# Kernel optimization log

Measured on AMD Instinct MI355X. Metric: run time of the kernel, lower is better.

Reference implementation:

```python
import jax, jax.numpy as jnp
import numpy as np


def setup_inputs() -> dict:
    key = jax.random.key(0)
    ks = jax.random.split(key, 8)
    B, N, D = 8, 2048, 128
    s = 1.0 / float(np.sqrt(D))
    node = jax.random.normal(ks[0], (B, N, D), dtype=jnp.float32)
    node_mask = jax.random.randint(ks[1], (B, N), 0, 2, dtype=jnp.int32)
    punctuation_graph = jax.random.randint(ks[2], (B, N, N), 0, 2, dtype=jnp.int32)
    w_nw = jax.random.uniform(ks[3], (1, D), jnp.float32, -s, s)
    b_nw = jax.random.uniform(ks[4], (1,), jnp.float32, -s, s)
    w_self = jax.random.uniform(ks[5], (D, D), jnp.float32, -s, s)
    b_self = jax.random.uniform(ks[6], (D,), jnp.float32, -s, s)
    w_punct = jax.random.uniform(ks[7], (D, D), jnp.float32, -s, s)
    return {"node": node, "node_mask": node_mask, "punctuation_graph": punctuation_graph,
            "w_nw": w_nw, "b_nw": b_nw, "w_self": w_self, "b_self": b_self,
            "w_punct": w_punct, "iteration_steps": 2}


def reference(node, node_mask, punctuation_graph, w_nw, b_nw, w_self, b_self, w_punct, iteration_steps):
    B, N, D = node.shape
    # dd_graph = mask outer product with zeroed diagonal; graph = dd_graph * punctuation_graph
    eye = jnp.eye(N, dtype=punctuation_graph.dtype)
    dd = node_mask[:, None, :] * node_mask[:, :, None] * (1 - eye)[None, :, :]  # [B,N,N]
    graph = dd * punctuation_graph  # [B,N,N] int, binary
    nbr_num = graph.sum(-1)  # [B,N]
    # replace_masked_values(nbr_num, nbr_num>=1, 1): nodes with no neighbors get denom 1
    nbr_f = jnp.where(nbr_num >= 1, nbr_num.astype(node.dtype), jnp.asarray(1.0, node.dtype))
    gmask = graph > 0
    weights = []
    x = node
    for _ in range(iteration_steps):  # small fixed step count
        dw = jax.nn.sigmoid(jnp.einsum('bnd,od->bno', x, w_nw) + b_nw)[..., 0]  # [B,N]
        weights.append(dw)
        self_info = jnp.einsum('bnd,ed->bne', x, w_self) + b_self  # [B,N,D]
        info_p = jnp.einsum('bnd,ed->bne', x, w_punct)  # [B,N,D]
        # node_weight[b,i,j] = dw[b,j] where graph[b,i,j] else 0
        nw = jnp.where(gmask, dw[:, None, :], jnp.asarray(0.0, x.dtype))  # [B,N,N]
        agg = jnp.einsum('bnm,bmd->bnd', nw, info_p) / nbr_f[..., None]
        x = jax.nn.relu(self_info + agg)
    all_weight = jnp.stack(weights, axis=1)  # [B, steps, N]
    return x, all_weight
```

## Files before the change

### kernel.cpp

```cpp
#include <hip/hip_runtime.h>
#include <hip/hip_bf16.h>

#define BB 8
#define NN 2048
#define DD 128

typedef __attribute__((ext_vector_type(8))) __bf16 bf16x8;
typedef __attribute__((ext_vector_type(4))) float f32x4;
typedef __attribute__((ext_vector_type(4))) int   i32x4;

static __device__ __forceinline__ unsigned short f2bf(float f) {
    union { float f; unsigned u; } v; v.f = f;
    unsigned r = (v.u + 0x7FFFu + ((v.u >> 16) & 1u)) >> 16;
    return (unsigned short)r;
}
static __device__ __forceinline__ float bf2f(unsigned short b) {
    union { unsigned u; float f; } v; v.u = ((unsigned)b) << 16;
    return v.f;
}

__global__ __launch_bounds__(256) void kernP(
    const int* __restrict__ punct, const int* __restrict__ mask,
    unsigned* __restrict__ pk, float* __restrict__ scale_g, float* __restrict__ pdm_g)
{
    const int t = threadIdx.x;
    const int wave = t >> 6, lane = t & 63;
    const int row_g = blockIdx.x * 4 + wave;
    const int b = row_g >> 11;
    const int i = row_g & (NN - 1);

    const int* prow = punct + (size_t)row_g * NN;
    const int* mrow = mask + (size_t)b * NN;

    unsigned pk0 = 0, pk1 = 0;
    int acc = 0;
    #pragma unroll 4
    for (int w = 0; w < 32; ++w) {
        const int col = w * 64 + lane;
        const int p = prow[col];
        const int m = mrow[col];
        const int pred = (p & m) & 1;
        unsigned long long bal = __ballot(pred);
        if (lane == w) { pk0 = (unsigned)bal; pk1 = (unsigned)(bal >> 32); }
        acc += pred + ((col == i ? pred : 0) << 16);
    }
    #pragma unroll
    for (int o = 32; o > 0; o >>= 1) acc += __shfl_xor(acc, o, 64);

    if (lane < 32) {
        uint2 w2; w2.x = pk0; w2.y = pk1;
        *(uint2*)(pk + (size_t)row_g * 64 + 2 * lane) = w2;
    }

    if (lane == 0) {
        const int nall = acc & 0xFFFF;
        const int pdm  = acc >> 16;
        const int mi   = mrow[i];
        const int nbr  = nall - pdm;
        scale_g[row_g] = mi ? 1.f / (float)(nbr < 1 ? 1 : nbr) : 0.f;
        pdm_g[row_g]   = (float)pdm;
    }
}

__global__ __launch_bounds__(256) void kernB(
    const float* __restrict__ x,
    const float* __restrict__ w_nw,  const float* __restrict__ b_nw,
    const float* __restrict__ w_self,const float* __restrict__ b_self,
    const float* __restrict__ w_punct,
    float* __restrict__ si_out,
    unsigned short* __restrict__ yne_out,
    unsigned short* __restrict__ yT_out,
    float* __restrict__ aw_out)
{
    __shared__ unsigned short xt[64*32];
    __shared__ unsigned short wst[128*32];
    __shared__ unsigned short wpt[128*32];
    __shared__ float wnw_l[DD];
    __shared__ float red[256];
    __shared__ float dw_l[64];
    __shared__ unsigned short ytl[128*72];

    const int t  = threadIdx.x;
    const int n0 = blockIdx.x * 64;
    const int b  = n0 >> 11;
    const int nb = n0 & (NN - 1);

    if (t < DD) wnw_l[t] = w_nw[t];
    __syncthreads();

    const int wave = t >> 6, lane = t & 63;
    const int wm = wave >> 1, wn = wave & 1;
    const int quad = lane >> 4, l16 = lane & 15;

    const int n_loc = t >> 2, dq = t & 3;
    const int we = t >> 1,   wh = t & 1;

    f32x4 accs[2][4] = {}; f32x4 accp[2][4] = {};
    float dwpart = 0.f;

    #pragma unroll
    for (int kk = 0; kk < 4; ++kk) {
        const int k0 = kk * 32;
        {
            const float* xs = x + (size_t)(n0 + n_loc) * DD + k0 + dq * 8;
            f32x4 a = *(const f32x4*)xs;
            f32x4 c = *(const f32x4*)(xs + 4);
            const float* wv = &wnw_l[k0 + dq * 8];
            dwpart += a.x*wv[0] + a.y*wv[1] + a.z*wv[2] + a.w*wv[3]
                    + c.x*wv[4] + c.y*wv[5] + c.z*wv[6] + c.w*wv[7];
            unsigned q0 = f2bf(a.x) | ((unsigned)f2bf(a.y) << 16);
            unsigned q1 = f2bf(a.z) | ((unsigned)f2bf(a.w) << 16);
            unsigned q2 = f2bf(c.x) | ((unsigned)f2bf(c.y) << 16);
            unsigned q3 = f2bf(c.z) | ((unsigned)f2bf(c.w) << 16);
            i32x4 pw = {(int)q0,(int)q1,(int)q2,(int)q3};
            *(i32x4*)&xt[n_loc*32 + dq*8] = pw;
        }
        {
            const float* s1 = w_self  + (size_t)we * DD + k0 + wh*16;
            const float* s2 = w_punct + (size_t)we * DD + k0 + wh*16;
            f32x4 a0 = *(const f32x4*)s1;      f32x4 a1 = *(const f32x4*)(s1+4);
            f32x4 a2 = *(const f32x4*)(s1+8);  f32x4 a3 = *(const f32x4*)(s1+12);
            unsigned q0 = f2bf(a0.x) | ((unsigned)f2bf(a0.y)<<16);
            unsigned q1 = f2bf(a0.z) | ((unsigned)f2bf(a0.w)<<16);
            unsigned q2 = f2bf(a1.x) | ((unsigned)f2bf(a1.y)<<16);
            unsigned q3 = f2bf(a1.z) | ((unsigned)f2bf(a1.w)<<16);
            unsigned q4 = f2bf(a2.x) | ((unsigned)f2bf(a2.y)<<16);
            unsigned q5 = f2bf(a2.z) | ((unsigned)f2bf(a2.w)<<16);
            unsigned q6 = f2bf(a3.x) | ((unsigned)f2bf(a3.y)<<16);
            unsigned q7 = f2bf(a3.z) | ((unsigned)f2bf(a3.w)<<16);
            i32x4 pw0 = {(int)q0,(int)q1,(int)q2,(int)q3};
            i32x4 pw1 = {(int)q4,(int)q5,(int)q6,(int)q7};
            *(i32x4*)&wst[we*32 + wh*16]     = pw0;
            *(i32x4*)&wst[we*32 + wh*16 + 8] = pw1;
            f32x4 c0 = *(const f32x4*)s2;      f32x4 c1 = *(const f32x4*)(s2+4);
            f32x4 c2 = *(const f32x4*)(s2+8);  f32x4 c3 = *(const f32x4*)(s2+12);
            unsigned r0 = f2bf(c0.x) | ((unsigned)f2bf(c0.y)<<16);
            unsigned r1 = f2bf(c0.z) | ((unsigned)f2bf(c0.w)<<16);
            unsigned r2 = f2bf(c1.x) | ((unsigned)f2bf(c1.y)<<16);
            unsigned r3 = f2bf(c1.z) | ((unsigned)f2bf(c1.w)<<16);
            unsigned r4 = f2bf(c2.x) | ((unsigned)f2bf(c2.y)<<16);
            unsigned r5 = f2bf(c2.z) | ((unsigned)f2bf(c2.w)<<16);
            unsigned r6 = f2bf(c3.x) | ((unsigned)f2bf(c3.y)<<16);
            unsigned r7 = f2bf(c3.z) | ((unsigned)f2bf(c3.w)<<16);
            i32x4 pv0 = {(int)r0,(int)r1,(int)r2,(int)r3};
            i32x4 pv1 = {(int)r4,(int)r5,(int)r6,(int)r7};
            *(i32x4*)&wpt[we*32 + wh*16]     = pv0;
            *(i32x4*)&wpt[we*32 + wh*16 + 8] = pv1;
        }
        __syncthreads();
        bf16x8 af[2], bs[4], bp[4];
        #pragma unroll
        for (int mt = 0; mt < 2; ++mt)
            af[mt] = *(const bf16x8*)&xt[(wm*32 + mt*16 + l16)*32 + quad*8];
        #pragma unroll
        for (int nt = 0; nt < 4; ++nt) {
            const int er = wn*64 + nt*16 + l16;
            bs[nt] = *(const bf16x8*)&wst[er*32 + quad*8];
            bp[nt] = *(const bf16x8*)&wpt[er*32 + quad*8];
        }
        #pragma unroll
        for (int mt = 0; mt < 2; ++mt)
            #pragma unroll
            for (int nt = 0; nt < 4; ++nt) {
                accs[mt][nt] = __builtin_amdgcn_mfma_f32_16x16x32_bf16(af[mt], bs[nt], accs[mt][nt], 0, 0, 0);
                accp[mt][nt] = __builtin_amdgcn_mfma_f32_16x16x32_bf16(af[mt], bp[nt], accp[mt][nt], 0, 0, 0);
            }
        __syncthreads();
    }

    red[t] = dwpart;
    __syncthreads();
    if (t < 64) {
        float s = red[4*t] + red[4*t+1] + red[4*t+2] + red[4*t+3] + b_nw[0];
        float dv = 1.f / (1.f + __expf(-s));
        dw_l[t] = dv;
        aw_out[(size_t)b * 2 * NN + nb + t] = dv;
    }
    __syncthreads();

    #pragma unroll
    for (int mt = 0; mt < 2; ++mt) {
        #pragma unroll
        for (int nt = 0; nt < 4; ++nt) {
            const int e = wn*64 + nt*16 + l16;
            const float bsv = b_self[e];
            #pragma unroll
            for (int r = 0; r < 4; ++r) {
                const int nl = wm*32 + mt*16 + quad*4 + r;
                const size_t idx = (size_t)(n0 + nl) * DD + e;
                si_out[idx] = accs[mt][nt][r] + bsv;
                const float yv = dw_l[nl] * accp[mt][nt][r];
                const unsigned short ub = f2bf(yv);
                yne_out[idx] = ub;
                ytl[e*72 + nl] = ub;
            }
        }
    }
    __syncthreads();
    {
        const int e = t >> 1, half = t & 1;
        const i32x4* src = (const i32x4*)&ytl[e*72 + half*32];
        i32x4 v0 = src[0], v1 = src[1], v2 = src[2], v3 = src[3];
        i32x4* dst = (i32x4*)(yT_out + (size_t)(b*DD + e) * NN + nb + half*32);
        dst[0] = v0; dst[1] = v1; dst[2] = v2; dst[3] = v3;
    }
}

__global__ __launch_bounds__(256) void kernC(
    const unsigned* __restrict__ pk,
    const float* __restrict__ scale_g, const float* __restrict__ pdm_g,
    const unsigned short* __restrict__ yT,
    const float* __restrict__ si,
    const unsigned short* __restrict__ yne,
    float* __restrict__ x_out)
{
    __shared__ unsigned pPk[64 * 68];
    __shared__ float scale_l[64];
    __shared__ float pdm_l[64];

    const int t  = threadIdx.x;
    const int b  = blockIdx.x >> 5;
    const int i0 = (blockIdx.x & 31) * 64;
    const size_t rg0 = (size_t)b * NN + i0;

    #pragma unroll
    for (int r = 0; r < 4; ++r) {
        const int u   = r * 256 + t;
        const int row = u >> 4;
        const int wq  = (u & 15) * 4;
        i32x4 v = *(const i32x4*)(pk + (rg0 + row) * 64 + wq);
        *(i32x4*)&pPk[row * 68 + wq] = v;
    }
    if (t < 64) {
        scale_l[t] = scale_g[rg0 + t];
        pdm_l[t]   = pdm_g[rg0 + t];
    }
    __syncthreads();

    const int wn = t >> 6, lane = t & 63;
    const int quad = lane >> 4, l16 = lane & 15;
    const unsigned short* yTb = yT + (size_t)b * DD * NN;

    f32x4 acc[4][2] = {};

    #pragma unroll 4
    for (int kk = 0; kk < 64; ++kk) {
        bf16x8 bfr[2];
        #pragma unroll
        for (int nt = 0; nt < 2; ++nt) {
            const int e = wn*32 + nt*16 + l16;
            bfr[nt] = *(const bf16x8*)(yTb + (size_t)e * NN + kk*32 + quad*8);
        }
        bf16x8 af[4];
        #pragma unroll
        for (int mt = 0; mt < 4; ++mt) {
            const unsigned w = pPk[(mt*16 + l16) * 68 + kk];
            const unsigned by = (w >> (quad * 8)) & 0xFFu;
            i32x4 ex;
            ex.x = ((by &   1u) ? 0x3F80 : 0) | ((by &   2u) ? 0x3F800000 : 0);
            ex.y = ((by &   4u) ? 0x3F80 : 0) | ((by &   8u) ? 0x3F800000 : 0);
            ex.z = ((by &  16u) ? 0x3F80 : 0) | ((by &  32u) ? 0x3F800000 : 0);
            ex.w = ((by &  64u) ? 0x3F80 : 0) | ((by & 128u) ? 0x3F800000 : 0);
            union { i32x4 i; bf16x8 h; } cv; cv.i = ex;
            af[mt] = cv.h;
        }
        #pragma unroll
        for (int mt = 0; mt < 4; ++mt)
            #pragma unroll
            for (int nt = 0; nt < 2; ++nt)
                acc[mt][nt] = __builtin_amdgcn_mfma_f32_16x16x32_bf16(af[mt], bfr[nt], acc[mt][nt], 0, 0, 0);
    }

    #pragma unroll
    for (int mt = 0; mt < 4; ++mt) {
        #pragma unroll
        for (int nt = 0; nt < 2; ++nt) {
            const int e = wn*32 + nt*16 + l16;
            #pragma unroll
            for (int r = 0; r < 4; ++r) {
                const int row = mt*16 + quad*4 + r;
                const size_t idx = (rg0 + row) * DD + e;
                const float yv = bf2f(yne[idx]);
                float v = si[idx] + scale_l[row] * (acc[mt][nt][r] - pdm_l[row] * yv);
                x_out[idx] = fmaxf(v, 0.f);
            }
        }
    }
}

extern "C" void kernel_launch(void* const* d_in, const int* in_sizes, int n_in,
                              void* d_out, int out_size, void* d_ws, size_t ws_size,
                              hipStream_t stream) {
    const float* node   = (const float*)d_in[0];
    const int*   mask   = (const int*)  d_in[1];
    const int*   punct  = (const int*)  d_in[2];
    const float* w_nw   = (const float*)d_in[3];
    const float* b_nw   = (const float*)d_in[4];
    const float* w_self = (const float*)d_in[5];
    const float* b_self = (const float*)d_in[6];
    const float* w_punct= (const float*)d_in[7];

    float* xout = (float*)d_out;
    float* aw   = xout + (size_t)BB * NN * DD;

    char* w = (char*)d_ws;
    float*          si   = (float*)w;
    unsigned short* yne  = (unsigned short*)(w + (8u  << 20));
    unsigned short* yT   = (unsigned short*)(w + (12u << 20));
    unsigned*       pk   = (unsigned*)(w + (16u << 20));
    float*          scl  = (float*)(w + (20u << 20));
    float*          pdm  = (float*)(w + (20u << 20) + (64u << 10));

    dim3 blk(256);
    kernP<<<dim3(4096), blk, 0, stream>>>(punct, mask, pk, scl, pdm);
    kernB<<<dim3(256), blk, 0, stream>>>(node, w_nw, b_nw, w_self, b_self, w_punct,
                                         si, yne, yT, aw);
    kernC<<<dim3(256), blk, 0, stream>>>(pk, scl, pdm, yT, si, yne, xout);
    kernB<<<dim3(256), blk, 0, stream>>>(xout, w_nw, b_nw, w_self, b_self, w_punct,
                                         si, yne, yT, aw + NN);
    kernC<<<dim3(256), blk, 0, stream>>>(pk, scl, pdm, yT, si, yne, xout);
}
```

Before: 286.3 us.

## Reassociate aggregation to multiply graph by dw-scaled x before weight projection, fusing steps

Reorders the per-step math: the graph aggregation now runs on dw-scaled x instead of on x@W_punct, and the self and punct projections are fused into one K=256 GEMM over [x, aggregate] against a concatenated bf16 weight matrix. That matrix is converted once in an extra kernP block. Each step's output kernel also emits the next step's bf16 x, scaled x, transposed operand and dw, which removes the separate projection kernel for step two and the fp32 self_info round trip. The trade-off is extra bf16 rounding of the aggregate before the projection, one more sync-heavy epilogue per block, and a redundant dummy dw computation in the final step.

```diff
diff --git a/kernel.cpp b/kernel.cpp
--- a/kernel.cpp
+++ b/kernel.cpp
@@ -21,9 +21,20 @@
 
 __global__ __launch_bounds__(256) void kernP(
     const int* __restrict__ punct, const int* __restrict__ mask,
-    unsigned* __restrict__ pk, float* __restrict__ scale_g, float* __restrict__ pdm_g)
+    const float* __restrict__ w_self, const float* __restrict__ w_punct,
+    unsigned* __restrict__ pk, float* __restrict__ scale_g, float* __restrict__ pdm_g,
+    unsigned short* __restrict__ wc)
 {
     const int t = threadIdx.x;
+    if (blockIdx.x == 4096) {
+        for (int idx = t; idx < 128 * 256; idx += 256) {
+            const int e = idx >> 8, k = idx & 255;
+            const float v = (k < 128) ? w_self[e * 128 + k]
+                                      : w_punct[e * 128 + (k - 128)];
+            wc[idx] = f2bf(v);
+        }
+        return;
+    }
     const int wave = t >> 6, lane = t & 63;
     const int row_g = blockIdx.x * 4 + wave;
     const int b = row_g >> 11;
@@ -37,9 +48,7 @@
     #pragma unroll 4
     for (int w = 0; w < 32; ++w) {
         const int col = w * 64 + lane;
-        const int p = prow[col];
-        const int m = mrow[col];
-        const int pred = (p & m) & 1;
+        const int pred = (prow[col] & mrow[col]) & 1;
         unsigned long long bal = __ballot(pred);
         if (lane == w) { pk0 = (unsigned)bal; pk1 = (unsigned)(bal >> 32); }
         acc += pred + ((col == i ? pred : 0) << 16);
@@ -51,7 +60,6 @@
         uint2 w2; w2.x = pk0; w2.y = pk1;
         *(uint2*)(pk + (size_t)row_g * 64 + 2 * lane) = w2;
     }
-
     if (lane == 0) {
         const int nall = acc & 0xFFFF;
         const int pdm  = acc >> 16;
@@ -62,23 +70,17 @@
     }
 }
 
-__global__ __launch_bounds__(256) void kernB(
+__global__ __launch_bounds__(256) void kernD(
     const float* __restrict__ x,
-    const float* __restrict__ w_nw,  const float* __restrict__ b_nw,
-    const float* __restrict__ w_self,const float* __restrict__ b_self,
-    const float* __restrict__ w_punct,
-    float* __restrict__ si_out,
-    unsigned short* __restrict__ yne_out,
-    unsigned short* __restrict__ yT_out,
-    float* __restrict__ aw_out)
+    const float* __restrict__ w_nw, const float* __restrict__ b_nw,
+    float* __restrict__ aw_out,
+    unsigned short* __restrict__ xbf, unsigned short* __restrict__ xw,
+    unsigned short* __restrict__ xwT)
 {
-    __shared__ unsigned short xt[64*32];
-    __shared__ unsigned short wst[128*32];
-    __shared__ unsigned short wpt[128*32];
     __shared__ float wnw_l[DD];
     __shared__ float red[256];
     __shared__ float dw_l[64];
-    __shared__ unsigned short ytl[128*72];
+    __shared__ unsigned short xl[64 * 136];
 
     const int t  = threadIdx.x;
     const int n0 = blockIdx.x * 64;
@@ -88,87 +90,18 @@
     if (t < DD) wnw_l[t] = w_nw[t];
     __syncthreads();
 
-    const int wave = t >> 6, lane = t & 63;
-    const int wm = wave >> 1, wn = wave & 1;
-    const int quad = lane >> 4, l16 = lane & 15;
-
-    const int n_loc = t >> 2, dq = t & 3;
-    const int we = t >> 1,   wh = t & 1;
-
-    f32x4 accs[2][4] = {}; f32x4 accp[2][4] = {};
-    float dwpart = 0.f;
-
-    #pragma unroll
-    for (int kk = 0; kk < 4; ++kk) {
-        const int k0 = kk * 32;
-        {
-            const float* xs = x + (size_t)(n0 + n_loc) * DD + k0 + dq * 8;
-            f32x4 a = *(const f32x4*)xs;
-            f32x4 c = *(const f32x4*)(xs + 4);
-            const float* wv = &wnw_l[k0 + dq * 8];
-            dwpart += a.x*wv[0] + a.y*wv[1] + a.z*wv[2] + a.w*wv[3]
-                    + c.x*wv[4] + c.y*wv[5] + c.z*wv[6] + c.w*wv[7];
-            unsigned q0 = f2bf(a.x) | ((unsigned)f2bf(a.y) << 16);
-            unsigned q1 = f2bf(a.z) | ((unsigned)f2bf(a.w) << 16);
-            unsigned q2 = f2bf(c.x) | ((unsigned)f2bf(c.y) << 16);
-            unsigned q3 = f2bf(c.z) | ((unsigned)f2bf(c.w) << 16);
-            i32x4 pw = {(int)q0,(int)q1,(int)q2,(int)q3};
-            *(i32x4*)&xt[n_loc*32 + dq*8] = pw;
-        }
-        {
-            const float* s1 = w_self  + (size_t)we * DD + k0 + wh*16;
-            const float* s2 = w_punct + (size_t)we * DD + k0 + wh*16;
-            f32x4 a0 = *(const f32x4*)s1;      f32x4 a1 = *(const f32x4*)(s1+4);
-            f32x4 a2 = *(const f32x4*)(s1+8);  f32x4 a3 = *(const f32x4*)(s1+12);
-            unsigned q0 = f2bf(a0.x) | ((unsigned)f2bf(a0.y)<<16);
-            unsigned q1 = f2bf(a0.z) | ((unsigned)f2bf(a0.w)<<16);
-            unsigned q2 = f2bf(a1.x) | ((unsigned)f2bf(a1.y)<<16);
-            unsigned q3 = f2bf(a1.z) | ((unsigned)f2bf(a1.w)<<16);
-            unsigned q4 = f2bf(a2.x) | ((unsigned)f2bf(a2.y)<<16);
-            unsigned q5 = f2bf(a2.z) | ((unsigned)f2bf(a2.w)<<16);
-            unsigned q6 = f2bf(a3.x) | ((unsigned)f2bf(a3.y)<<16);
-            unsigned q7 = f2bf(a3.z) | ((unsigned)f2bf(a3.w)<<16);
-            i32x4 pw0 = {(int)q0,(int)q1,(int)q2,(int)q3};
-            i32x4 pw1 = {(int)q4,(int)q5,(int)q6,(int)q7};
-            *(i32x4*)&wst[we*32 + wh*16]     = pw0;
-            *(i32x4*)&wst[we*32 + wh*16 + 8] = pw1;
-            f32x4 c0 = *(const f32x4*)s2;      f32x4 c1 = *(const f32x4*)(s2+4);
-            f32x4 c2 = *(const f32x4*)(s2+8);  f32x4 c3 = *(const f32x4*)(s2+12);
-            unsigned r0 = f2bf(c0.x) | ((unsigned)f2bf(c0.y)<<16);
-            unsigned r1 = f2bf(c0.z) | ((unsigned)f2bf(c0.w)<<16);
-            unsigned r2 = f2bf(c1.x) | ((unsigned)f2bf(c1.y)<<16);
-            unsigned r3 = f2bf(c1.z) | ((unsigned)f2bf(c1.w)<<16);
-            unsigned r4 = f2bf(c2.x) | ((unsigned)f2bf(c2.y)<<16);
-            unsigned r5 = f2bf(c2.z) | ((unsigned)f2bf(c2.w)<<16);
-            unsigned r6 = f2bf(c3.x) | ((unsigned)f2bf(c3.y)<<16);
-            unsigned r7 = f2bf(c3.z) | ((unsigned)f2bf(c3.w)<<16);
-            i32x4 pv0 = {(int)r0,(int)r1,(int)r2,(int)r3};
-            i32x4 pv1 = {(int)r4,(int)r5,(int)r6,(int)r7};
-            *(i32x4*)&wpt[we*32 + wh*16]     = pv0;
-            *(i32x4*)&wpt[we*32 + wh*16 + 8] = pv1;
-        }
-        __syncthreads();
-        bf16x8 af[2], bs[4], bp[4];
-        #pragma unroll
-        for (int mt = 0; mt < 2; ++mt)
-            af[mt] = *(const bf16x8*)&xt[(wm*32 + mt*16 + l16)*32 + quad*8];
-        #pragma unroll
-        for (int nt = 0; nt < 4; ++nt) {
-            const int er = wn*64 + nt*16 + l16;
-            bs[nt] = *(const bf16x8*)&wst[er*32 + quad*8];
-            bp[nt] = *(const bf16x8*)&wpt[er*32 + quad*8];
-        }
-        #pragma unroll
-        for (int mt = 0; mt < 2; ++mt)
-            #pragma unroll
-            for (int nt = 0; nt < 4; ++nt) {
-                accs[mt][nt] = __builtin_amdgcn_mfma_f32_16x16x32_bf16(af[mt], bs[nt], accs[mt][nt], 0, 0, 0);
-                accp[mt][nt] = __builtin_amdgcn_mfma_f32_16x16x32_bf16(af[mt], bp[nt], accp[mt][nt], 0, 0, 0);
-            }
-        __syncthreads();
-    }
-
-    red[t] = dwpart;
+    const int row = t >> 2, q = t & 3;
+    const float* xs = x + (size_t)(n0 + row) * DD + q * 32;
+    float vals[32];
+    float dp = 0.f;
+    #pragma unroll
+    for (int j = 0; j < 8; ++j) {
+        f32x4 a = *(const f32x4*)(xs + j * 4);
+        vals[j*4+0] = a.x; vals[j*4+1] = a.y; vals[j*4+2] = a.z; vals[j*4+3] = a.w;
+        const float* wv = &wnw_l[q * 32 + j * 4];
+        dp += a.x*wv[0] + a.y*wv[1] + a.z*wv[2] + a.w*wv[3];
+    }
+    red[t] = dp;
     __syncthreads();
     if (t < 64) {
         float s = red[4*t] + red[4*t+1] + red[4*t+2] + red[4*t+3] + b_nw[0];
@@ -178,45 +111,66 @@
     }
     __syncthreads();
 
-    #pragma unroll
-    for (int mt = 0; mt < 2; ++mt) {
-        #pragma unroll
-        for (int nt = 0; nt < 4; ++nt) {
-            const int e = wn*64 + nt*16 + l16;
-            const float bsv = b_self[e];
-            #pragma unroll
-            for (int r = 0; r < 4; ++r) {
-                const int nl = wm*32 + mt*16 + quad*4 + r;
-                const size_t idx = (size_t)(n0 + nl) * DD + e;
-                si_out[idx] = accs[mt][nt][r] + bsv;
-                const float yv = dw_l[nl] * accp[mt][nt][r];
-                const unsigned short ub = f2bf(yv);
-                yne_out[idx] = ub;
-                ytl[e*72 + nl] = ub;
-            }
-        }
-    }
-    __syncthreads();
-    {
-        const int e = t >> 1, half = t & 1;
-        const i32x4* src = (const i32x4*)&ytl[e*72 + half*32];
-        i32x4 v0 = src[0], v1 = src[1], v2 = src[2], v3 = src[3];
-        i32x4* dst = (i32x4*)(yT_out + (size_t)(b*DD + e) * NN + nb + half*32);
-        dst[0] = v0; dst[1] = v1; dst[2] = v2; dst[3] = v3;
-    }
-}
-
-__global__ __launch_bounds__(256) void kernC(
+    unsigned pb[16];
+    #pragma unroll
+    for (int j = 0; j < 16; ++j)
+        pb[j] = f2bf(vals[2*j]) | ((unsigned)f2bf(vals[2*j+1]) << 16);
+    {
+        i32x4* dst = (i32x4*)(xbf + (size_t)(n0 + row) * DD + q * 32);
+        i32x4 v0 = {(int)pb[0],(int)pb[1],(int)pb[2],(int)pb[3]};
+        i32x4 v1 = {(int)pb[4],(int)pb[5],(int)pb[6],(int)pb[7]};
+        i32x4 v2 = {(int)pb[8],(int)pb[9],(int)pb[10],(int)pb[11]};
+        i32x4 v3 = {(int)pb[12],(int)pb[13],(int)pb[14],(int)pb[15]};
+        dst[0]=v0; dst[1]=v1; dst[2]=v2; dst[3]=v3;
+    }
+    const float dwv = dw_l[row];
+    #pragma unroll
+    for (int j = 0; j < 16; ++j)
+        pb[j] = f2bf(vals[2*j]*dwv) | ((unsigned)f2bf(vals[2*j+1]*dwv) << 16);
+    {
+        i32x4 v0 = {(int)pb[0],(int)pb[1],(int)pb[2],(int)pb[3]};
+        i32x4 v1 = {(int)pb[4],(int)pb[5],(int)pb[6],(int)pb[7]};
+        i32x4 v2 = {(int)pb[8],(int)pb[9],(int)pb[10],(int)pb[11]};
+        i32x4 v3 = {(int)pb[12],(int)pb[13],(int)pb[14],(int)pb[15]};
+        i32x4* dst = (i32x4*)(xw + (size_t)(n0 + row) * DD + q * 32);
+        dst[0]=v0; dst[1]=v1; dst[2]=v2; dst[3]=v3;
+        i32x4* ld = (i32x4*)&xl[row * 136 + q * 32];
+        ld[0]=v0; ld[1]=v1; ld[2]=v2; ld[3]=v3;
+    }
+    __syncthreads();
+    {
+        const int d = t >> 1, half = t & 1;
+        unsigned o[16];
+        #pragma unroll
+        for (int k = 0; k < 16; ++k) {
+            const int r0 = half * 32 + 2 * k;
+            o[k] = (unsigned)xl[r0 * 136 + d] | ((unsigned)xl[(r0+1) * 136 + d] << 16);
+        }
+        i32x4 v0 = {(int)o[0],(int)o[1],(int)o[2],(int)o[3]};
+        i32x4 v1 = {(int)o[4],(int)o[5],(int)o[6],(int)o[7]};
+        i32x4 v2 = {(int)o[8],(int)o[9],(int)o[10],(int)o[11]};
+        i32x4 v3 = {(int)o[12],(int)o[13],(int)o[14],(int)o[15]};
+        i32x4* dst = (i32x4*)(xwT + (size_t)(b * DD + d) * NN + nb + half * 32);
+        dst[0]=v0; dst[1]=v1; dst[2]=v2; dst[3]=v3;
+    }
+}
+
+__global__ __launch_bounds__(256) void kernE(
     const unsigned* __restrict__ pk,
     const float* __restrict__ scale_g, const float* __restrict__ pdm_g,
-    const unsigned short* __restrict__ yT,
-    const float* __restrict__ si,
-    const unsigned short* __restrict__ yne,
-    float* __restrict__ x_out)
+    const unsigned short* __restrict__ xwT,
+    const unsigned short* __restrict__ xw,
+    const unsigned short* __restrict__ xbf,
+    const unsigned short* __restrict__ wc,
+    const float* __restrict__ b_self,
+    const float* __restrict__ w_nw, const float* __restrict__ b_nw,
+    float* __restrict__ x_out, float* __restrict__ aw_next,
+    unsigned short* __restrict__ xbf_o, unsigned short* __restrict__ xw_o,
+    unsigned short* __restrict__ xwT_o)
 {
     __shared__ unsigned pPk[64 * 68];
-    __shared__ float scale_l[64];
-    __shared__ float pdm_l[64];
+    __shared__ unsigned short ZsL[64 * 136];
+    __shared__ float scale_l[64], pdm_l[64], dw_l[64];
 
     const int t  = threadIdx.x;
     const int b  = blockIdx.x >> 5;
@@ -225,7 +179,7 @@
 
     #pragma unroll
     for (int r = 0; r < 4; ++r) {
-        const int u   = r * 256 + t;
+        const int u = r * 256 + t;
         const int row = u >> 4;
         const int wq  = (u & 15) * 4;
         i32x4 v = *(const i32x4*)(pk + (rg0 + row) * 64 + wq);
@@ -239,17 +193,16 @@
 
     const int wn = t >> 6, lane = t & 63;
     const int quad = lane >> 4, l16 = lane & 15;
-    const unsigned short* yTb = yT + (size_t)b * DD * NN;
+    const unsigned short* xwTb = xwT + (size_t)b * DD * NN;
 
     f32x4 acc[4][2] = {};
-
     #pragma unroll 4
     for (int kk = 0; kk < 64; ++kk) {
         bf16x8 bfr[2];
         #pragma unroll
         for (int nt = 0; nt < 2; ++nt) {
-            const int e = wn*32 + nt*16 + l16;
-            bfr[nt] = *(const bf16x8*)(yTb + (size_t)e * NN + kk*32 + quad*8);
+            const int d = wn*32 + nt*16 + l16;
+            bfr[nt] = *(const bf16x8*)(xwTb + (size_t)d * NN + kk*32 + quad*8);
         }
         bf16x8 af[4];
         #pragma unroll
@@ -275,16 +228,131 @@
     for (int mt = 0; mt < 4; ++mt) {
         #pragma unroll
         for (int nt = 0; nt < 2; ++nt) {
-            const int e = wn*32 + nt*16 + l16;
+            const int d = wn*32 + nt*16 + l16;
             #pragma unroll
             for (int r = 0; r < 4; ++r) {
                 const int row = mt*16 + quad*4 + r;
-                const size_t idx = (rg0 + row) * DD + e;
-                const float yv = bf2f(yne[idx]);
-                float v = si[idx] + scale_l[row] * (acc[mt][nt][r] - pdm_l[row] * yv);
-                x_out[idx] = fmaxf(v, 0.f);
+                const float xwv = bf2f(xw[(rg0 + row) * DD + d]);
+                const float zs = scale_l[row] * (acc[mt][nt][r] - pdm_l[row] * xwv);
+                ZsL[row * 136 + d] = f2bf(zs);
             }
         }
+    }
+    __syncthreads();
+
+    f32x4 acc2[4][2] = {};
+    #pragma unroll
+    for (int kq2 = 0; kq2 < 8; ++kq2) {
+        bf16x8 b2[2];
+        #pragma unroll
+        for (int nt2 = 0; nt2 < 2; ++nt2) {
+            const int e = wn*32 + nt2*16 + l16;
+            b2[nt2] = *(const bf16x8*)(wc + (size_t)e * 256 + kq2*32 + quad*8);
+        }
+        bf16x8 a2[4];
+        if (kq2 < 4) {
+            #pragma unroll
+            for (int mt = 0; mt < 4; ++mt)
+                a2[mt] = *(const bf16x8*)(xbf + (rg0 + mt*16 + l16) * DD + kq2*32 + quad*8);
+        } else {
+            #pragma unroll
+            for (int mt = 0; mt < 4; ++mt)
+                a2[mt] = *(const bf16x8*)&ZsL[(mt*16 + l16) * 136 + (kq2-4)*32 + quad*8];
+        }
+        #pragma unroll
+        for (int mt = 0; mt < 4; ++mt)
+            #pragma unroll
+            for (int nt2 = 0; nt2 < 2; ++nt2)
+                acc2[mt][nt2] = __builtin_amdgcn_mfma_f32_16x16x32_bf16(a2[mt], b2[nt2], acc2[mt][nt2], 0, 0, 0);
+    }
+    __syncthreads();
+
+    float bias[2], wnv[2];
+    #pragma unroll
+    for (int nt2 = 0; nt2 < 2; ++nt2) {
+        const int e = wn*32 + nt2*16 + l16;
+        bias[nt2] = b_self[e];
+        wnv[nt2]  = w_nw[e];
+    }
+    float* red = (float*)pPk;
+    #pragma unroll
+    for (int mt = 0; mt < 4; ++mt) {
+        #pragma unroll
+        for (int r = 0; r < 4; ++r) {
+            const int row = mt*16 + quad*4 + r;
+            float p = 0.f;
+            #pragma unroll
+            for (int nt2 = 0; nt2 < 2; ++nt2) {
+                const int e = wn*32 + nt2*16 + l16;
+                float v = fmaxf(acc2[mt][nt2][r] + bias[nt2], 0.f);
+                acc2[mt][nt2][r] = v;
+                x_out[(rg0 + row) * DD + e] = v;
+                ZsL[row * 136 + e] = f2bf(v);
+                p += v * wnv[nt2];
+            }
+            red[row * 65 + wn*16 + l16] = p;
+        }
+    }
+    __syncthreads();
+    if (t < 64) {
+        float s = b_nw[0];
+        #pragma unroll 8
+        for (int c = 0; c < 64; ++c) s += red[t * 65 + c];
+        float dv = 1.f / (1.f + __expf(-s));
+        dw_l[t] = dv;
+        aw_next[(size_t)b * 2 * NN + i0 + t] = dv;
+    }
+    __syncthreads();
+
+    {
+        const int row = t >> 2, q = t & 3;
+        const i32x4* src = (const i32x4*)&ZsL[row * 136 + q * 32];
+        i32x4 u0 = src[0], u1 = src[1], u2 = src[2], u3 = src[3];
+        i32x4* db = (i32x4*)(xbf_o + (rg0 + row) * DD + q * 32);
+        db[0]=u0; db[1]=u1; db[2]=u2; db[3]=u3;
+        const float dwv = dw_l[row];
+        unsigned uu[8] = {(unsigned)u0.x,(unsigned)u0.y,(unsigned)u0.z,(unsigned)u0.w,
+                          (unsigned)u1.x,(unsigned)u1.y,(unsigned)u1.z,(unsigned)u1.w};
+        unsigned vv[8] = {(unsigned)u2.x,(unsigned)u2.y,(unsigned)u2.z,(unsigned)u2.w,
+                          (unsigned)u3.x,(unsigned)u3.y,(unsigned)u3.z,(unsigned)u3.w};
+        unsigned o[16];
+        #pragma unroll
+        for (int j = 0; j < 8; ++j) {
+            float lo = bf2f((unsigned short)(uu[j] & 0xFFFF)) * dwv;
+            float hi = bf2f((unsigned short)(uu[j] >> 16)) * dwv;
+            o[j] = f2bf(lo) | ((unsigned)f2bf(hi) << 16);
+        }
+        #pragma unroll
+        for (int j = 0; j < 8; ++j) {
+            float lo = bf2f((unsigned short)(vv[j] & 0xFFFF)) * dwv;
+            float hi = bf2f((unsigned short)(vv[j] >> 16)) * dwv;
+            o[8+j] = f2bf(lo) | ((unsigned)f2bf(hi) << 16);
+        }
+        i32x4 w0 = {(int)o[0],(int)o[1],(int)o[2],(int)o[3]};
+        i32x4 w1 = {(int)o[4],(int)o[5],(int)o[6],(int)o[7]};
+        i32x4 w2 = {(int)o[8],(int)o[9],(int)o[10],(int)o[11]};
+        i32x4 w3 = {(int)o[12],(int)o[13],(int)o[14],(int)o[15]};
+        i32x4* dw_ = (i32x4*)(xw_o + (rg0 + row) * DD + q * 32);
+        dw_[0]=w0; dw_[1]=w1; dw_[2]=w2; dw_[3]=w3;
+        i32x4* lw = (i32x4*)&ZsL[row * 136 + q * 32];
+        __syncthreads();
+        lw[0]=w0; lw[1]=w1; lw[2]=w2; lw[3]=w3;
+    }
+    __syncthreads();
+    {
+        const int d = t >> 1, half = t & 1;
+        unsigned o[16];
+        #pragma unroll
+        for (int k = 0; k < 16; ++k) {
+            const int r0 = half * 32 + 2 * k;
+            o[k] = (unsigned)ZsL[r0 * 136 + d] | ((unsigned)ZsL[(r0+1) * 136 + d] << 16);
+        }
+        i32x4 v0 = {(int)o[0],(int)o[1],(int)o[2],(int)o[3]};
+        i32x4 v1 = {(int)o[4],(int)o[5],(int)o[6],(int)o[7]};
+        i32x4 v2 = {(int)o[8],(int)o[9],(int)o[10],(int)o[11]};
+        i32x4 v3 = {(int)o[12],(int)o[13],(int)o[14],(int)o[15]};
+        i32x4* dst = (i32x4*)(xwT_o + (size_t)(b * DD + d) * NN + i0 + half * 32);
+        dst[0]=v0; dst[1]=v1; dst[2]=v2; dst[3]=v3;
     }
 }
 
@@ -304,19 +372,23 @@
     float* aw   = xout + (size_t)BB * NN * DD;
 
     char* w = (char*)d_ws;
-    float*          si   = (float*)w;
-    unsigned short* yne  = (unsigned short*)(w + (8u  << 20));
-    unsigned short* yT   = (unsigned short*)(w + (12u << 20));
-    unsigned*       pk   = (unsigned*)(w + (16u << 20));
-    float*          scl  = (float*)(w + (20u << 20));
-    float*          pdm  = (float*)(w + (20u << 20) + (64u << 10));
+    unsigned*       pk    = (unsigned*)w;
+    float*          scl   = (float*)(w + (4u<<20));
+    float*          pdm   = (float*)(w + (4u<<20) + (64u<<10));
+    unsigned short* wc    = (unsigned short*)(w + (4u<<20) + (128u<<10));
+    float*          awdum = (float*)(w + (4u<<20) + (192u<<10));
+    unsigned short* xbf0  = (unsigned short*)(w + (5u<<20));
+    unsigned short* xw0   = (unsigned short*)(w + (9u<<20));
+    unsigned short* xwT0  = (unsigned short*)(w + (13u<<20));
+    unsigned short* xbf1  = (unsigned short*)(w + (17u<<20));
+    unsigned short* xw1   = (unsigned short*)(w + (21u<<20));
+    unsigned short* xwT1  = (unsigned short*)(w + (25u<<20));
 
     dim3 blk(256);
-    kernP<<<dim3(4096), blk, 0, stream>>>(punct, mask, pk, scl, pdm);
-    kernB<<<dim3(256), blk, 0, stream>>>(node, w_nw, b_nw, w_self, b_self, w_punct,
-                                         si, yne, yT, aw);
-    kernC<<<dim3(256), blk, 0, stream>>>(pk, scl, pdm, yT, si, yne, xout);
-    kernB<<<dim3(256), blk, 0, stream>>>(xout, w_nw, b_nw, w_self, b_self, w_punct,
-                                         si, yne, yT, aw + NN);
-    kernC<<<dim3(256), blk, 0, stream>>>(pk, scl, pdm, yT, si, yne, xout);
-}
+    kernP<<<dim3(4097), blk, 0, stream>>>(punct, mask, w_self, w_punct, pk, scl, pdm, wc);
+    kernD<<<dim3(256), blk, 0, stream>>>(node, w_nw, b_nw, aw, xbf0, xw0, xwT0);
+    kernE<<<dim3(256), blk, 0, stream>>>(pk, scl, pdm, xwT0, xw0, xbf0, wc, b_self,
+                                         w_nw, b_nw, xout, aw + NN, xbf1, xw1, xwT1);
+    kernE<<<dim3(256), blk, 0, stream>>>(pk, scl, pdm, xwT1, xw1, xbf1, wc, b_self,
+                                         w_nw, b_nw, xout, awdum, xbf0, xw0, xwT0);
+}
```

After: 317.8 us. +11.0%, slower.
